# Kernel tuning notes

Measured on AMD Instinct MI355X. Metric: run time of the kernel, lower is better.

Reference implementation:

```python
import jax, jax.numpy as jnp
import numpy as np

D_MODEL = 512
N_HEADS = 8
N_KV_HEADS = 2
HEAD_DIM = 64
PITCH_VOCAB = 128


def setup_inputs() -> dict:
    key = jax.random.key(0)
    ks = jax.random.split(key, 6)
    B, T, P = 2, 256, 12
    s = lambda fan_in: 1.0 / np.sqrt(fan_in)
    hidden_states = jax.random.normal(ks[0], (B, T, P, D_MODEL), dtype=jnp.float32)
    Wq = jax.random.normal(ks[1], (D_MODEL, N_HEADS * HEAD_DIM), dtype=jnp.float32) * s(D_MODEL)
    Wk = jax.random.normal(ks[2], (D_MODEL, N_KV_HEADS * HEAD_DIM), dtype=jnp.float32) * s(D_MODEL)
    Wv = jax.random.normal(ks[3], (D_MODEL, N_KV_HEADS * HEAD_DIM), dtype=jnp.float32) * s(D_MODEL)
    Wo = jax.random.normal(ks[4], (N_HEADS * HEAD_DIM, D_MODEL), dtype=jnp.float32) * s(N_HEADS * HEAD_DIM)
    pitch_table = jax.random.normal(ks[5], (PITCH_VOCAB, HEAD_DIM), dtype=jnp.float32)
    return {"hidden_states": hidden_states, "Wq": Wq, "Wk": Wk, "Wv": Wv, "Wo": Wo, "pitch_table": pitch_table}


def reference(hidden_states, Wq, Wk, Wv, Wo, pitch_table):
    B, T, P, C = hidden_states.shape
    H, Hkv, d = N_HEADS, N_KV_HEADS, HEAD_DIM
    rep = H // Hkv

    q = (hidden_states @ Wq).reshape(B, T, P, H, d)
    k = (hidden_states @ Wk).reshape(B, T, P, Hkv, d)
    v = (hidden_states @ Wv).reshape(B, T, P, Hkv, d)

    # GQA repeat_kv: (B,T,P,Hkv,d) -> (B,T,P,H,d)
    k = jnp.repeat(k, rep, axis=3)
    v = jnp.repeat(v, rep, axis=3)

    # additive pitch bias on q and k
    pitch_emb = pitch_table[jnp.arange(P)]  # (P, d)
    bias = pitch_emb[None, None, :, None, :]
    q = q + bias
    k = k + bias

    # flatten (T,P) -> S and move heads forward: (B,H,S,d)
    S = T * P
    q = q.transpose(0, 3, 1, 2, 4).reshape(B, H, S, d)
    k = k.transpose(0, 3, 1, 2, 4).reshape(B, H, S, d)
    v = v.transpose(0, 3, 1, 2, 4).reshape(B, H, S, d)

    scale = 1.0 / jnp.sqrt(jnp.asarray(d, dtype=q.dtype))
    attn = jax.nn.softmax(jnp.einsum('bhqd,bhkd->bhqk', q, k) * scale, axis=-1)
    out = jnp.einsum('bhqk,bhkd->bhqd', attn, v)  # (B,H,S,d)

    out = out.reshape(B, H, T, P, d).transpose(0, 2, 3, 1, 4).reshape(B, T, P, H * d)
    return out @ Wo
```

## Files before the change

kernel.cpp:

```cpp
#include <hip/hip_runtime.h>
#include <hip/hip_fp16.h>

#define B_   2
#define T_   256
#define P_   12
#define C_   512
#define H_   8
#define HKV_ 2
#define D_   64
#define S_   (T_ * P_)
#define M_   (B_ * S_)
#define NQKV 768

typedef _Float16 half8_t __attribute__((ext_vector_type(8)));
typedef _Float16 half4_t __attribute__((ext_vector_type(4)));
typedef _Float16 half2_t __attribute__((ext_vector_type(2)));
typedef float    float4_t __attribute__((ext_vector_type(4)));

#if __has_builtin(__builtin_amdgcn_exp2f)
#define EXP2(x) __builtin_amdgcn_exp2f(x)
#else
#define EXP2(x) __expf((x) * 0.69314718f)
#endif

#define SOFT_SHIFT 20.0f
#define SOFT_CLAMP2 15.5f
#define QSCALE (0.125f * 1.44269504f)

#define GLDS16(gp, lp)                                                          \
    __builtin_amdgcn_global_load_lds(                                           \
        (const __attribute__((address_space(1))) void*)(gp),                    \
        (__attribute__((address_space(3))) void*)(lp), 16, 0, 0)

__global__ __launch_bounds__(256) void prep_kernel(
    const float* __restrict__ hs,
    const float* __restrict__ Wq, const float* __restrict__ Wk,
    const float* __restrict__ Wv, const float* __restrict__ Wo,
    _Float16* __restrict__ hs16,
    _Float16* __restrict__ wcatT,
    _Float16* __restrict__ woT)
{
    const int blk = blockIdx.x;
    const int tid = threadIdx.x;

    if (blk < 160) {
        __shared__ __attribute__((aligned(16))) _Float16 Ts[64][72];
        int t, K;
        const float* src; int srcN, col0; _Float16* dst;
        if (blk < 96) { t = blk; K = 512; dst = wcatT;
            int nt = t / 8;
            int kt = t % 8;
            int n0 = nt * 64, k0 = kt * 64;
            if (n0 < 512)      { src = Wq; srcN = 512; col0 = n0; }
            else if (n0 < 640) { src = Wk; srcN = 128; col0 = n0 - 512; }
            else               { src = Wv; srcN = 128; col0 = n0 - 640; }
#pragma unroll
            for (int i = 0; i < 4; ++i) {
                int row = i * 16 + (tid >> 4);
                int cg  = tid & 15;
                float4_t v = *(const float4_t*)(src + (size_t)(k0 + row) * srcN + col0 + cg * 4);
                Ts[cg * 4 + 0][row] = (_Float16)v[0];
                Ts[cg * 4 + 1][row] = (_Float16)v[1];
                Ts[cg * 4 + 2][row] = (_Float16)v[2];
                Ts[cg * 4 + 3][row] = (_Float16)v[3];
            }
            __syncthreads();
#pragma unroll
            for (int i = 0; i < 2; ++i) {
                int seg = i * 256 + tid;
                int row = seg >> 3, s = seg & 7;
                *(half8_t*)(dst + (size_t)(n0 + row) * K + k0 + s * 8) =
                    *(const half8_t*)&Ts[row][s * 8];
            }
        } else { t = blk - 96; K = 512; dst = woT;
            int nt = t / 8, kt = t % 8;
            int n0 = nt * 64, k0 = kt * 64;
#pragma unroll
            for (int i = 0; i < 4; ++i) {
                int row = i * 16 + (tid >> 4);
                int cg  = tid & 15;
                float4_t v = *(const float4_t*)(Wo + (size_t)(k0 + row) * 512 + n0 + cg * 4);
                Ts[cg * 4 + 0][row] = (_Float16)v[0];
                Ts[cg * 4 + 1][row] = (_Float16)v[1];
                Ts[cg * 4 + 2][row] = (_Float16)v[2];
                Ts[cg * 4 + 3][row] = (_Float16)v[3];
            }
            __syncthreads();
#pragma unroll
            for (int i = 0; i < 2; ++i) {
                int seg = i * 256 + tid;
                int row = seg >> 3, s = seg & 7;
                *(half8_t*)(dst + (size_t)(n0 + row) * K + k0 + s * 8) =
                    *(const half8_t*)&Ts[row][s * 8];
            }
        }
    } else {
        int base = (blk - 160) * 4096;
#pragma unroll
        for (int i = 0; i < 16; ++i) {
            int f4 = base + i * 256 + tid;
            float4_t v = *(const float4_t*)(hs + (size_t)f4 * 4);
            half4_t hv;
            hv[0] = (_Float16)v[0]; hv[1] = (_Float16)v[1];
            hv[2] = (_Float16)v[2]; hv[3] = (_Float16)v[3];
            *(half4_t*)(hs16 + (size_t)f4 * 4) = hv;
        }
    }
}

__global__ __launch_bounds__(256) void qkv_kernel(
    const _Float16* __restrict__ A,
    const _Float16* __restrict__ WT,
    const float* __restrict__ pitch,
    _Float16* __restrict__ qb,
    _Float16* __restrict__ kb,
    _Float16* __restrict__ vb)
{
    const int m0   = blockIdx.x * 64;
    const int n0   = blockIdx.y * 64;
    const int tid  = threadIdx.x;
    const int wave = tid >> 6;
    const int lane = tid & 63;
    const int ln   = lane & 15;
    const int quad = lane >> 4;

    __shared__ __attribute__((aligned(16))) _Float16 gs[16384];

    float4_t acc[4];
#pragma unroll
    for (int nt = 0; nt < 4; ++nt) acc[nt] = (float4_t){0.f, 0.f, 0.f, 0.f};

    const int srow = wave * 8 + (lane >> 3);
    const int sg   = (lane & 7) ^ (lane >> 3);
    const _Float16* Asrc = A  + (size_t)(m0 + srow) * 512 + sg * 8;
    const _Float16* Bsrc = WT + (size_t)(n0 + srow) * 512 + sg * 8;
    _Float16* const awd = gs + wave * 512;
    _Float16* const bwd = gs + 8192 + wave * 512;

#define QKV_STAGE(buf, k0)                                        \
    do {                                                          \
        GLDS16(Asrc + (k0),         awd + (buf) * 4096);          \
        GLDS16(Asrc + (k0) + 16384, awd + (buf) * 4096 + 2048);   \
        GLDS16(Bsrc + (k0),         bwd + (buf) * 4096);          \
        GLDS16(Bsrc + (k0) + 16384, bwd + (buf) * 4096 + 2048);   \
    } while (0)

    const int colx = (ln & 7) << 3;

    QKV_STAGE(0, 0);
    asm volatile("s_waitcnt vmcnt(0)" ::: "memory");
    __syncthreads();

#pragma unroll
    for (int kk = 0; kk < 8; ++kk) {
        const int cur = kk & 1;
        if (kk < 7) QKV_STAGE(cur ^ 1, (kk + 1) * 64);

#pragma unroll
        for (int ks = 0; ks < 2; ++ks) {
            half8_t afrag = *(const half8_t*)&gs[cur * 4096 +
                (wave * 16 + ln) * 64 + ((ks * 32 + quad * 8) ^ colx)];
#pragma unroll
            for (int nt = 0; nt < 4; ++nt) {
                half8_t bfrag = *(const half8_t*)&gs[8192 + cur * 4096 +
                    (nt * 16 + ln) * 64 + ((ks * 32 + quad * 8) ^ colx)];
                acc[nt] = __builtin_amdgcn_mfma_f32_16x16x32_f16(afrag, bfrag, acc[nt], 0, 0, 0);
            }
        }

        if (kk < 7) {
            asm volatile("s_waitcnt vmcnt(0)" ::: "memory");
            __syncthreads();
        }
    }
#undef QKV_STAGE

    const int bb      = m0 / S_;
    const int s00     = m0 - bb * S_;
    const int sl_base = wave * 16 + quad * 4;
    const int s_base  = s00 + sl_base;
    const int p_base  = s_base % P_;

    if (n0 < 512) {
        const int h = n0 >> 6;
#pragma unroll
        for (int r = 0; r < 4; ++r) {
            int p = p_base + r; if (p >= P_) p -= P_;
            const float* pr = pitch + p * 64;
            size_t rowb = ((size_t)(bb * H_ + h) * S_ + s_base + r) * 64;
#pragma unroll
            for (int nt = 0; nt < 4; ++nt) {
                int dd = nt * 16 + ln;
                float v = (acc[nt][r] + pr[dd]) * QSCALE;
                qb[rowb + dd] = (_Float16)v;
            }
        }
    } else if (n0 < 640) {
        const int h = (n0 - 512) >> 6;
#pragma unroll
        for (int r = 0; r < 4; ++r) {
            int p = p_base + r; if (p >= P_) p -= P_;
            const float* pr = pitch + p * 64;
            size_t rowb = ((size_t)(bb * HKV_ + h) * S_ + s_base + r) * 64;
#pragma unroll
            for (int nt = 0; nt < 4; ++nt) {
                int dd = nt * 16 + ln;
                kb[rowb + dd] = (_Float16)(acc[nt][r] + pr[dd]);
            }
        }
    } else {
        const int h = (n0 - 640) >> 6;
        __syncthreads();
#pragma unroll
        for (int nt = 0; nt < 4; ++nt)
#pragma unroll
            for (int r = 0; r < 4; ++r)
                gs[(nt * 16 + ln) * 64 + ((sl_base + r) ^ ((ln & 7) << 3))] =
                    (_Float16)acc[nt][r];
        __syncthreads();
        const int rw = tid >> 2;
        const int c0 = (tid & 3) * 16;
        const int rx = (rw & 7) << 3;
        _Float16* dst = vb + ((size_t)(bb * HKV_ + h) * 64 + rw) * S_ + s00 + c0;
        *(half8_t*)dst       = *(const half8_t*)&gs[rw * 64 + (c0 ^ rx)];
        *(half8_t*)(dst + 8) = *(const half8_t*)&gs[rw * 64 + ((c0 + 8) ^ rx)];
    }
}

__global__ __launch_bounds__(512) void attn_kernel(
    const _Float16* __restrict__ qbuf,
    const _Float16* __restrict__ kbuf,
    const _Float16* __restrict__ vtb,
    _Float16* __restrict__ ob)
{
    const int qblk = blockIdx.x;
    const int bh   = blockIdx.y;
    const int b    = bh >> 3;
    const int h    = bh & 7;
    const int hkv  = h >> 2;
    const int tid  = threadIdx.x;
    const int w    = tid >> 6;
    const int lane = tid & 63;
    const int ln   = lane & 15;
    const int quad = lane >> 4;

    const _Float16* Q  = qbuf + ((size_t)(b * H_ + h)) * S_ * 64;
    const _Float16* K  = kbuf + ((size_t)(b * HKV_ + hkv)) * S_ * 64;
    const _Float16* Vt = vtb  + ((size_t)(b * HKV_ + hkv)) * 64 * S_;

    __shared__ __attribute__((aligned(16))) _Float16 Ks[128][80];
    __shared__ __attribute__((aligned(16))) _Float16 VT[64][136];
    __shared__ __attribute__((aligned(16))) _Float16 Ps[8][16][40];

    const int qbase = qblk * 64 + (w & 3) * 16;
    const int kk0   = (w >> 2) * 32;

    half8_t qfrag[2];
#pragma unroll
    for (int ks = 0; ks < 2; ++ks)
        qfrag[ks] = *(const half8_t*)&Q[(size_t)(qbase + ln) * 64 + ks * 32 + quad * 8];

    float4_t o[4];
#pragma unroll
    for (int nt = 0; nt < 4; ++nt) o[nt] = (float4_t){0.f, 0.f, 0.f, 0.f};
    float lr[4] = {0.f, 0.f, 0.f, 0.f};

    const int j = tid >> 3, s = tid & 7;
    const int r0 = ((j & 1) << 4) | ((j >> 5) << 5) | ((j >> 1) & 15);

    half8_t kr0, kr1, vr0, vr1;
    kr0 = *(const half8_t*)&K[(size_t)j * 64 + s * 8];
    kr1 = *(const half8_t*)&K[(size_t)(64 + j) * 64 + s * 8];
    vr0 = *(const half8_t*)&Vt[(size_t)j * S_ + s * 8];
    vr1 = *(const half8_t*)&Vt[(size_t)j * S_ + 64 + s * 8];

    for (int kt = 0; kt < S_; kt += 128) {
        __syncthreads();
        *(half8_t*)&Ks[r0][s * 8]      = kr0;
        *(half8_t*)&Ks[r0 + 64][s * 8] = kr1;
        *(half8_t*)&VT[j][s * 8]       = vr0;
        *(half8_t*)&VT[j][64 + s * 8]  = vr1;
        __syncthreads();

        if (kt + 128 < S_) {
            kr0 = *(const half8_t*)&K[(size_t)(kt + 128 + j) * 64 + s * 8];
            kr1 = *(const half8_t*)&K[(size_t)(kt + 128 + 64 + j) * 64 + s * 8];
            vr0 = *(const half8_t*)&Vt[(size_t)j * S_ + kt + 128 + s * 8];
            vr1 = *(const half8_t*)&Vt[(size_t)j * S_ + kt + 128 + 64 + s * 8];
        }

#pragma unroll
        for (int h2 = 0; h2 < 2; ++h2) {
            const int kb = h2 * 64 + kk0;

            float4_t sf[2];
            __builtin_amdgcn_s_setprio(1);
#pragma unroll
            for (int c = 0; c < 2; ++c) {
                sf[c] = (float4_t){-SOFT_SHIFT, -SOFT_SHIFT, -SOFT_SHIFT, -SOFT_SHIFT};
#pragma unroll
                for (int ks = 0; ks < 2; ++ks) {
                    half8_t kf = *(const half8_t*)&Ks[kb + c * 16 + ln][ks * 32 + quad * 8];
                    sf[c] = __builtin_amdgcn_mfma_f32_16x16x32_f16(qfrag[ks], kf, sf[c], 0, 0, 0);
                }
            }
            __builtin_amdgcn_s_setprio(0);

#pragma unroll
            for (int rr = 0; rr < 4; ++rr) {
                float p0 = EXP2(fminf(sf[0][rr], SOFT_CLAMP2));
                float p1 = EXP2(fminf(sf[1][rr], SOFT_CLAMP2));
                lr[rr] += p0 + p1;
                half2_t w2; w2[0] = (_Float16)p0; w2[1] = (_Float16)p1;
                *(half2_t*)&Ps[w][quad * 4 + rr][2 * ln] = w2;
            }

            half8_t pf = *(const half8_t*)&Ps[w][ln][quad * 8];
            __builtin_amdgcn_s_setprio(1);
#pragma unroll
            for (int nt = 0; nt < 4; ++nt) {
                half8_t vf = *(const half8_t*)&VT[nt * 16 + ln][kb + quad * 8];
                o[nt] = __builtin_amdgcn_mfma_f32_16x16x32_f16(pf, vf, o[nt], 0, 0, 0);
            }
            __builtin_amdgcn_s_setprio(0);
        }
    }

    __syncthreads();
    if (w >= 4) {
        float* od = (float*)&Ks[0][0] + (w - 4) * 1280;
#pragma unroll
        for (int nt = 0; nt < 4; ++nt)
            *(float4_t*)&od[lane * 20 + nt * 4] = o[nt];
        float* ld = (float*)&Ps[0][0][0] + (w - 4) * 256;
        *(float4_t*)&ld[lane * 4] = (float4_t){lr[0], lr[1], lr[2], lr[3]};
    }
    __syncthreads();
    if (w < 4) {
        const float* os = (const float*)&Ks[0][0] + w * 1280;
        const float* ls = (const float*)&Ps[0][0][0] + w * 256;
        float4_t ls4 = *(const float4_t*)&ls[lane * 4];
        float4_t os4[4];
#pragma unroll
        for (int nt = 0; nt < 4; ++nt)
            os4[nt] = *(const float4_t*)&os[lane * 20 + nt * 4];
#pragma unroll
        for (int rr = 0; rr < 4; ++rr) {
            float l = lr[rr] + ls4[rr];
            l += __shfl_xor(l, 1);
            l += __shfl_xor(l, 2);
            l += __shfl_xor(l, 4);
            l += __shfl_xor(l, 8);
            float inv = 1.0f / l;
            int qg = qbase + quad * 4 + rr;
            size_t base = ((size_t)(b * S_ + qg)) * 512 + h * 64;
#pragma unroll
            for (int nt = 0; nt < 4; ++nt) {
                float vsum = o[nt][rr] + os4[nt][rr];
                ob[base + nt * 16 + ln] = (_Float16)(vsum * inv);
            }
        }
    }
}

__global__ __launch_bounds__(256) void proj_out_kernel(
    const _Float16* __restrict__ A,
    const _Float16* __restrict__ WT,
    float* __restrict__ outp)
{
    const int m0   = blockIdx.x * 64;
    const int n0   = blockIdx.y * 64;
    const int tid  = threadIdx.x;
    const int wave = tid >> 6;
    const int lane = tid & 63;
    const int ln   = lane & 15;
    const int quad = lane >> 4;

    __shared__ __attribute__((aligned(16))) _Float16 gs[16384];

    float4_t acc[4];
#pragma unroll
    for (int nt = 0; nt < 4; ++nt) acc[nt] = (float4_t){0.f, 0.f, 0.f, 0.f};

    const int srow = wave * 8 + (lane >> 3);
    const int sg   = (lane & 7) ^ (lane >> 3);
    const _Float16* Asrc = A  + (size_t)(m0 + srow) * 512 + sg * 8;
    const _Float16* Bsrc = WT + (size_t)(n0 + srow) * 512 + sg * 8;
    _Float16* const awd = gs + wave * 512;
    _Float16* const bwd = gs + 8192 + wave * 512;

#define PRJ_STAGE(buf, k0)                                        \
    do {                                                          \
        GLDS16(Asrc + (k0),         awd + (buf) * 4096);          \
        GLDS16(Asrc + (k0) + 16384, awd + (buf) * 4096 + 2048);   \
        GLDS16(Bsrc + (k0),         bwd + (buf) * 4096);          \
        GLDS16(Bsrc + (k0) + 16384, bwd + (buf) * 4096 + 2048);   \
    } while (0)

    const int colx = (ln & 7) << 3;

    PRJ_STAGE(0, 0);
    asm volatile("s_waitcnt vmcnt(0)" ::: "memory");
    __syncthreads();

#pragma unroll
    for (int kk = 0; kk < 8; ++kk) {
        const int cur = kk & 1;
        if (kk < 7) PRJ_STAGE(cur ^ 1, (kk + 1) * 64);

#pragma unroll
        for (int ks = 0; ks < 2; ++ks) {
            half8_t afrag = *(const half8_t*)&gs[cur * 4096 +
                (wave * 16 + ln) * 64 + ((ks * 32 + quad * 8) ^ colx)];
#pragma unroll
            for (int nt = 0; nt < 4; ++nt) {
                half8_t bfrag = *(const half8_t*)&gs[8192 + cur * 4096 +
                    (nt * 16 + ln) * 64 + ((ks * 32 + quad * 8) ^ colx)];
                acc[nt] = __builtin_amdgcn_mfma_f32_16x16x32_f16(afrag, bfrag, acc[nt], 0, 0, 0);
            }
        }

        if (kk < 7) {
            asm volatile("s_waitcnt vmcnt(0)" ::: "memory");
            __syncthreads();
        }
    }
#undef PRJ_STAGE

#pragma unroll
    for (int nt = 0; nt < 4; ++nt) {
        int n = n0 + nt * 16 + ln;
#pragma unroll
        for (int r = 0; r < 4; ++r) {
            int m = m0 + wave * 16 + quad * 4 + r;
            outp[(size_t)m * 512 + n] = acc[nt][r];
        }
    }
}

extern "C" void kernel_launch(void* const* d_in, const int* in_sizes, int n_in,
                              void* d_out, int out_size, void* d_ws, size_t ws_size,
                              hipStream_t stream) {
    const float* hs    = (const float*)d_in[0];
    const float* Wq    = (const float*)d_in[1];
    const float* Wk    = (const float*)d_in[2];
    const float* Wv    = (const float*)d_in[3];
    const float* Wo    = (const float*)d_in[4];
    const float* pitch = (const float*)d_in[5];
    float* out = (float*)d_out;

    _Float16* hs16  = (_Float16*)d_ws;
    _Float16* o_buf = hs16;
    _Float16* q_buf = hs16 + (size_t)M_ * 512;
    _Float16* k_buf = q_buf + (size_t)B_ * H_ * S_ * 64;
    _Float16* v_buf = k_buf + (size_t)B_ * HKV_ * S_ * 64;
    _Float16* wcatT = v_buf + (size_t)B_ * HKV_ * S_ * 64;
    _Float16* woT   = wcatT + (size_t)NQKV * 512;

    prep_kernel<<<352, 256, 0, stream>>>(hs, Wq, Wk, Wv, Wo, hs16, wcatT, woT);
    qkv_kernel<<<dim3(M_ / 64, NQKV / 64), 256, 0, stream>>>(hs16, wcatT, pitch, q_buf, k_buf, v_buf);
    attn_kernel<<<dim3(S_ / 64, B_ * H_), 512, 0, stream>>>(q_buf, k_buf, v_buf, o_buf);
    proj_out_kernel<<<dim3(M_ / 64, 8), 256, 0, stream>>>(o_buf, woT, out);
}
```

Measured before the change: 162.3 us.

## Fuse fp32-to-fp16 hidden-state conversion into QKV GEMM operand loads

The separate pass that converted hidden_states to fp16 in prep_kernel is removed. qkv_kernel now loads fp32 rows directly, converts them in registers and writes them to swizzled LDS, while B tiles keep using async global_load_lds. This drops a full write and re-read of the converted activation buffer. The cost is that each of the 12 N-column blocks reloads the fp32 A tile at twice the bytes and adds register pressure in the GEMM loop. Separately, the attention epilogue's cross-wave reduction buffer changes from stride 20 to stride 16 with scalar LDS accesses.

New measurement: 158.5 us. -2.4%, faster.

```diff
diff --git a/kernel.cpp b/kernel.cpp
--- a/kernel.cpp
+++ b/kernel.cpp
@@ -32,84 +32,77 @@
         (const __attribute__((address_space(1))) void*)(gp),                    \
         (__attribute__((address_space(3))) void*)(lp), 16, 0, 0)
 
+__device__ __forceinline__ half8_t cvt8(float4_t u0, float4_t u1) {
+    half8_t h;
+    h[0] = (_Float16)u0[0]; h[1] = (_Float16)u0[1];
+    h[2] = (_Float16)u0[2]; h[3] = (_Float16)u0[3];
+    h[4] = (_Float16)u1[0]; h[5] = (_Float16)u1[1];
+    h[6] = (_Float16)u1[2]; h[7] = (_Float16)u1[3];
+    return h;
+}
+
 __global__ __launch_bounds__(256) void prep_kernel(
-    const float* __restrict__ hs,
     const float* __restrict__ Wq, const float* __restrict__ Wk,
     const float* __restrict__ Wv, const float* __restrict__ Wo,
-    _Float16* __restrict__ hs16,
     _Float16* __restrict__ wcatT,
     _Float16* __restrict__ woT)
 {
     const int blk = blockIdx.x;
     const int tid = threadIdx.x;
 
-    if (blk < 160) {
-        __shared__ __attribute__((aligned(16))) _Float16 Ts[64][72];
-        int t, K;
-        const float* src; int srcN, col0; _Float16* dst;
-        if (blk < 96) { t = blk; K = 512; dst = wcatT;
-            int nt = t / 8;
-            int kt = t % 8;
-            int n0 = nt * 64, k0 = kt * 64;
-            if (n0 < 512)      { src = Wq; srcN = 512; col0 = n0; }
-            else if (n0 < 640) { src = Wk; srcN = 128; col0 = n0 - 512; }
-            else               { src = Wv; srcN = 128; col0 = n0 - 640; }
-#pragma unroll
-            for (int i = 0; i < 4; ++i) {
-                int row = i * 16 + (tid >> 4);
-                int cg  = tid & 15;
-                float4_t v = *(const float4_t*)(src + (size_t)(k0 + row) * srcN + col0 + cg * 4);
-                Ts[cg * 4 + 0][row] = (_Float16)v[0];
-                Ts[cg * 4 + 1][row] = (_Float16)v[1];
-                Ts[cg * 4 + 2][row] = (_Float16)v[2];
-                Ts[cg * 4 + 3][row] = (_Float16)v[3];
-            }
-            __syncthreads();
-#pragma unroll
-            for (int i = 0; i < 2; ++i) {
-                int seg = i * 256 + tid;
-                int row = seg >> 3, s = seg & 7;
-                *(half8_t*)(dst + (size_t)(n0 + row) * K + k0 + s * 8) =
-                    *(const half8_t*)&Ts[row][s * 8];
-            }
-        } else { t = blk - 96; K = 512; dst = woT;
-            int nt = t / 8, kt = t % 8;
-            int n0 = nt * 64, k0 = kt * 64;
-#pragma unroll
-            for (int i = 0; i < 4; ++i) {
-                int row = i * 16 + (tid >> 4);
-                int cg  = tid & 15;
-                float4_t v = *(const float4_t*)(Wo + (size_t)(k0 + row) * 512 + n0 + cg * 4);
-                Ts[cg * 4 + 0][row] = (_Float16)v[0];
-                Ts[cg * 4 + 1][row] = (_Float16)v[1];
-                Ts[cg * 4 + 2][row] = (_Float16)v[2];
-                Ts[cg * 4 + 3][row] = (_Float16)v[3];
-            }
-            __syncthreads();
-#pragma unroll
-            for (int i = 0; i < 2; ++i) {
-                int seg = i * 256 + tid;
-                int row = seg >> 3, s = seg & 7;
-                *(half8_t*)(dst + (size_t)(n0 + row) * K + k0 + s * 8) =
-                    *(const half8_t*)&Ts[row][s * 8];
-            }
+    __shared__ __attribute__((aligned(16))) _Float16 Ts[64][72];
+    if (blk < 96) {
+        int nt = blk / 8, kt = blk % 8;
+        int n0 = nt * 64, k0 = kt * 64;
+        const float* src; int srcN, col0;
+        if (n0 < 512)      { src = Wq; srcN = 512; col0 = n0; }
+        else if (n0 < 640) { src = Wk; srcN = 128; col0 = n0 - 512; }
+        else               { src = Wv; srcN = 128; col0 = n0 - 640; }
+#pragma unroll
+        for (int i = 0; i < 4; ++i) {
+            int row = i * 16 + (tid >> 4);
+            int cg  = tid & 15;
+            float4_t v = *(const float4_t*)(src + (size_t)(k0 + row) * srcN + col0 + cg * 4);
+            Ts[cg * 4 + 0][row] = (_Float16)v[0];
+            Ts[cg * 4 + 1][row] = (_Float16)v[1];
+            Ts[cg * 4 + 2][row] = (_Float16)v[2];
+            Ts[cg * 4 + 3][row] = (_Float16)v[3];
+        }
+        __syncthreads();
+#pragma unroll
+        for (int i = 0; i < 2; ++i) {
+            int seg = i * 256 + tid;
+            int row = seg >> 3, s = seg & 7;
+            *(half8_t*)(wcatT + (size_t)(n0 + row) * 512 + k0 + s * 8) =
+                *(const half8_t*)&Ts[row][s * 8];
         }
     } else {
-        int base = (blk - 160) * 4096;
-#pragma unroll
-        for (int i = 0; i < 16; ++i) {
-            int f4 = base + i * 256 + tid;
-            float4_t v = *(const float4_t*)(hs + (size_t)f4 * 4);
-            half4_t hv;
-            hv[0] = (_Float16)v[0]; hv[1] = (_Float16)v[1];
-            hv[2] = (_Float16)v[2]; hv[3] = (_Float16)v[3];
-            *(half4_t*)(hs16 + (size_t)f4 * 4) = hv;
+        int t = blk - 96;
+        int nt = t / 8, kt = t % 8;
+        int n0 = nt * 64, k0 = kt * 64;
+#pragma unroll
+        for (int i = 0; i < 4; ++i) {
+            int row = i * 16 + (tid >> 4);
+            int cg  = tid & 15;
+            float4_t v = *(const float4_t*)(Wo + (size_t)(k0 + row) * 512 + n0 + cg * 4);
+            Ts[cg * 4 + 0][row] = (_Float16)v[0];
+            Ts[cg * 4 + 1][row] = (_Float16)v[1];
+            Ts[cg * 4 + 2][row] = (_Float16)v[2];
+            Ts[cg * 4 + 3][row] = (_Float16)v[3];
+        }
+        __syncthreads();
+#pragma unroll
+        for (int i = 0; i < 2; ++i) {
+            int seg = i * 256 + tid;
+            int row = seg >> 3, s = seg & 7;
+            *(half8_t*)(woT + (size_t)(n0 + row) * 512 + k0 + s * 8) =
+                *(const half8_t*)&Ts[row][s * 8];
         }
     }
 }
 
 __global__ __launch_bounds__(256) void qkv_kernel(
-    const _Float16* __restrict__ A,
+    const float* __restrict__ A32,
     const _Float16* __restrict__ WT,
     const float* __restrict__ pitch,
     _Float16* __restrict__ qb,
@@ -130,31 +123,48 @@
 #pragma unroll
     for (int nt = 0; nt < 4; ++nt) acc[nt] = (float4_t){0.f, 0.f, 0.f, 0.f};
 
-    const int srow = wave * 8 + (lane >> 3);
-    const int sg   = (lane & 7) ^ (lane >> 3);
-    const _Float16* Asrc = A  + (size_t)(m0 + srow) * 512 + sg * 8;
-    const _Float16* Bsrc = WT + (size_t)(n0 + srow) * 512 + sg * 8;
-    _Float16* const awd = gs + wave * 512;
+    const int brow = wave * 8 + (lane >> 3);
+    const int bg   = (lane & 7) ^ (lane >> 3);
+    const _Float16* Bsrc = WT + (size_t)(n0 + brow) * 512 + bg * 8;
     _Float16* const bwd = gs + 8192 + wave * 512;
 
-#define QKV_STAGE(buf, k0)                                        \
+#define STAGE_B(buf, k0)                                          \
     do {                                                          \
-        GLDS16(Asrc + (k0),         awd + (buf) * 4096);          \
-        GLDS16(Asrc + (k0) + 16384, awd + (buf) * 4096 + 2048);   \
         GLDS16(Bsrc + (k0),         bwd + (buf) * 4096);          \
         GLDS16(Bsrc + (k0) + 16384, bwd + (buf) * 4096 + 2048);   \
     } while (0)
 
+    const int asr = tid >> 3;
+    const int ass = tid & 7;
+    const int awz = (ass ^ (asr & 7)) * 8;
+
     const int colx = (ln & 7) << 3;
 
-    QKV_STAGE(0, 0);
+    half8_t ar[2];
+
+    STAGE_B(0, 0);
+#pragma unroll
+    for (int i = 0; i < 2; ++i) {
+        const float* p = A32 + (size_t)(m0 + i * 32 + asr) * 512 + ass * 8;
+        ar[i] = cvt8(*(const float4_t*)p, *(const float4_t*)(p + 4));
+    }
+#pragma unroll
+    for (int i = 0; i < 2; ++i)
+        *(half8_t*)&gs[(i * 32 + asr) * 64 + awz] = ar[i];
     asm volatile("s_waitcnt vmcnt(0)" ::: "memory");
     __syncthreads();
 
 #pragma unroll
     for (int kk = 0; kk < 8; ++kk) {
         const int cur = kk & 1;
-        if (kk < 7) QKV_STAGE(cur ^ 1, (kk + 1) * 64);
+        if (kk < 7) {
+            STAGE_B(cur ^ 1, (kk + 1) * 64);
+#pragma unroll
+            for (int i = 0; i < 2; ++i) {
+                const float* p = A32 + (size_t)(m0 + i * 32 + asr) * 512 + (kk + 1) * 64 + ass * 8;
+                ar[i] = cvt8(*(const float4_t*)p, *(const float4_t*)(p + 4));
+            }
+        }
 
 #pragma unroll
         for (int ks = 0; ks < 2; ++ks) {
@@ -169,11 +179,14 @@
         }
 
         if (kk < 7) {
+#pragma unroll
+            for (int i = 0; i < 2; ++i)
+                *(half8_t*)&gs[(cur ^ 1) * 4096 + (i * 32 + asr) * 64 + awz] = ar[i];
             asm volatile("s_waitcnt vmcnt(0)" ::: "memory");
             __syncthreads();
         }
     }
-#undef QKV_STAGE
+#undef STAGE_B
 
     const int bb      = m0 / S_;
     const int s00     = m0 - bb * S_;
@@ -328,25 +341,22 @@
 
     __syncthreads();
     if (w >= 4) {
-        float* od = (float*)&Ks[0][0] + (w - 4) * 1280;
+        float* od = (float*)&Ks[0][0] + (w - 4) * 1024;
 #pragma unroll
         for (int nt = 0; nt < 4; ++nt)
-            *(float4_t*)&od[lane * 20 + nt * 4] = o[nt];
+            *(float4_t*)&od[lane * 16 + nt * 4] = o[nt];
         float* ld = (float*)&Ps[0][0][0] + (w - 4) * 256;
-        *(float4_t*)&ld[lane * 4] = (float4_t){lr[0], lr[1], lr[2], lr[3]};
+#pragma unroll
+        for (int rr = 0; rr < 4; ++rr)
+            ld[lane * 4 + rr] = lr[rr];
     }
     __syncthreads();
     if (w < 4) {
-        const float* os = (const float*)&Ks[0][0] + w * 1280;
+        const float* os = (const float*)&Ks[0][0] + w * 1024;
         const float* ls = (const float*)&Ps[0][0][0] + w * 256;
-        float4_t ls4 = *(const float4_t*)&ls[lane * 4];
-        float4_t os4[4];
-#pragma unroll
-        for (int nt = 0; nt < 4; ++nt)
-            os4[nt] = *(const float4_t*)&os[lane * 20 + nt * 4];
 #pragma unroll
         for (int rr = 0; rr < 4; ++rr) {
-            float l = lr[rr] + ls4[rr];
+            float l = lr[rr] + ls[lane * 4 + rr];
             l += __shfl_xor(l, 1);
             l += __shfl_xor(l, 2);
             l += __shfl_xor(l, 4);
@@ -356,7 +366,7 @@
             size_t base = ((size_t)(b * S_ + qg)) * 512 + h * 64;
 #pragma unroll
             for (int nt = 0; nt < 4; ++nt) {
-                float vsum = o[nt][rr] + os4[nt][rr];
+                float vsum = o[nt][rr] + os[lane * 16 + nt * 4 + rr];
                 ob[base + nt * 16 + ln] = (_Float16)(vsum * inv);
             }
         }
@@ -449,16 +459,15 @@
     const float* pitch = (const float*)d_in[5];
     float* out = (float*)d_out;
 
-    _Float16* hs16  = (_Float16*)d_ws;
-    _Float16* o_buf = hs16;
-    _Float16* q_buf = hs16 + (size_t)M_ * 512;
+    _Float16* o_buf = (_Float16*)d_ws;
+    _Float16* q_buf = o_buf + (size_t)M_ * 512;
     _Float16* k_buf = q_buf + (size_t)B_ * H_ * S_ * 64;
     _Float16* v_buf = k_buf + (size_t)B_ * HKV_ * S_ * 64;
     _Float16* wcatT = v_buf + (size_t)B_ * HKV_ * S_ * 64;
     _Float16* woT   = wcatT + (size_t)NQKV * 512;
 
-    prep_kernel<<<352, 256, 0, stream>>>(hs, Wq, Wk, Wv, Wo, hs16, wcatT, woT);
-    qkv_kernel<<<dim3(M_ / 64, NQKV / 64), 256, 0, stream>>>(hs16, wcatT, pitch, q_buf, k_buf, v_buf);
+    prep_kernel<<<160, 256, 0, stream>>>(Wq, Wk, Wv, Wo, wcatT, woT);
+    qkv_kernel<<<dim3(M_ / 64, NQKV / 64), 256, 0, stream>>>(hs, wcatT, pitch, q_buf, k_buf, v_buf);
     attn_kernel<<<dim3(S_ / 64, B_ * H_), 512, 0, stream>>>(q_buf, k_buf, v_buf, o_buf);
     proj_out_kernel<<<dim3(M_ / 64, 8), 256, 0, stream>>>(o_buf, woT, out);
 }
```
